# Optimization experiments

Hardware: AMD Instinct MI355X
Metric: run time of the kernel (lower is better)

## Reference

```python
import jax, jax.numpy as jnp
import numpy as np


def setup_inputs() -> dict:
    key = jax.random.key(0)
    k1, k2 = jax.random.split(key)
    B, C_in, H, Wd = 8, 64, 64, 64
    C_a = 32
    x = jax.random.normal(k1, (B, C_in, H, Wd), dtype=jnp.float32)
    # 1x1 conv == per-pixel linear map: weight [C_a, C_in], bias [C_a]
    W = jax.random.normal(k2, (C_a, C_in), dtype=jnp.float32) * (1.0 / np.sqrt(C_in))
    b = jnp.zeros((C_a,), dtype=jnp.float32)
    return {"x": x, "W": W, "b": b}


def reference(x, W, b):
    B, C, H, Wd = x.shape
    N = H * Wd
    # g = 1x1 conv: [B, C_a, H, W] -> flatten spatial -> [B, C_a, N]
    g = jnp.einsum('oc,bchw->bohw', W, x) + b[None, :, None, None]
    g = g.reshape(B, -1, N)
    # alpha[b, n, m] = softmax_m( sum_c g[b,c,n] * g[b,c,m] )  (unscaled)
    scores = jnp.einsum('bcn,bcm->bnm', g, g)
    alpha = jax.nn.softmax(scores, axis=2)
    # r[b, c, n] = sum_m alpha[b,n,m] * x[b,c,m]
    xf = x.reshape(B, C, N)
    r = jnp.einsum('bnm,bcm->bcn', alpha, xf)
    # residual (intended semantics of is_residual=True) + ReLU epilogue
    r = r + xf
    out = jax.nn.relu(r).reshape(B, C, H, Wd)
    return (out, alpha)
```

## Files before the change

kernel.cpp:

```cpp
#include <hip/hip_runtime.h>
#include <math.h>

#define BB 8
#define CC 64
#define NA 4096
#define KA 32
#define LOG2E 1.4426950408889634f

typedef short bfrag __attribute__((ext_vector_type(8)));
typedef int   i4    __attribute__((ext_vector_type(4)));
typedef float f4    __attribute__((ext_vector_type(4)));
typedef float f16v  __attribute__((ext_vector_type(16)));

__device__ __forceinline__ f16v mf(bfrag a, bfrag b, f16v c) {
    return __builtin_amdgcn_mfma_f32_32x32x16_bf16(a, b, c, 0, 0, 0);
}

__device__ __forceinline__ unsigned short bfrne(float f) {
    unsigned u = __builtin_bit_cast(unsigned, f);
    return (unsigned short)((u + 0x7FFFu + ((u >> 16) & 1u)) >> 16);
}
__device__ __forceinline__ unsigned pk2(float a, float b) {
    return (unsigned)bfrne(a) | ((unsigned)bfrne(b) << 16);
}
__device__ __forceinline__ float bf2f(unsigned short h) {
    unsigned u = ((unsigned)h) << 16;
    return __builtin_bit_cast(float, u);
}

__global__ __launch_bounds__(256) void k_g(const float* __restrict__ x,
                                           const float* __restrict__ W,
                                           const float* __restrict__ bias,
                                           short* __restrict__ ghi,
                                           short* __restrict__ glo,
                                           float* __restrict__ norms,
                                           int* __restrict__ gmaxi,
                                           float* __restrict__ lsum) {
    __shared__ float Wl[KA * CC];
    __shared__ float bl[KA];
    __shared__ float red[4];
    int tid = threadIdx.x;
    for (int i = tid; i < KA * CC; i += 256) Wl[i] = W[i];
    if (tid < KA) bl[tid] = bias[tid];
    __syncthreads();

    int b = blockIdx.y;
    int n = blockIdx.x * 256 + tid;

    float acc[KA];
#pragma unroll
    for (int k = 0; k < KA; k++) acc[k] = 0.f;

    const float* xp = x + (size_t)b * CC * NA + n;
#pragma unroll 4
    for (int c = 0; c < CC; c++) {
        float xv = xp[(size_t)c * NA];
#pragma unroll
        for (int k = 0; k < KA; k++) acc[k] = fmaf(Wl[k * CC + c], xv, acc[k]);
    }

    float ss = 0.f;
    unsigned ph[KA / 2], pl[KA / 2];
#pragma unroll
    for (int k = 0; k < KA; k += 2) {
        float v0 = acc[k] + bl[k];
        float v1 = acc[k + 1] + bl[k + 1];
        ss = fmaf(v0, v0, fmaf(v1, v1, ss));
        unsigned short h0 = bfrne(v0), h1 = bfrne(v1);
        float l0 = v0 - bf2f(h0), l1 = v1 - bf2f(h1);
        ph[k / 2] = (unsigned)h0 | ((unsigned)h1 << 16);
        pl[k / 2] = (unsigned)bfrne(l0) | ((unsigned)bfrne(l1) << 16);
    }
    float nrm = sqrtf(ss);
    norms[b * NA + n] = nrm;
    lsum[b * NA + n] = 0.f;

    size_t row = ((size_t)b * NA + n) * KA;
#pragma unroll
    for (int q = 0; q < 4; q++) {
        i4 vh = { (int)ph[4 * q], (int)ph[4 * q + 1], (int)ph[4 * q + 2], (int)ph[4 * q + 3] };
        i4 vl = { (int)pl[4 * q], (int)pl[4 * q + 1], (int)pl[4 * q + 2], (int)pl[4 * q + 3] };
        *(i4*)(ghi + row + q * 8) = vh;
        *(i4*)(glo + row + q * 8) = vl;
    }

    float m = nrm;
#pragma unroll
    for (int off = 1; off < 64; off <<= 1) m = fmaxf(m, __shfl_xor(m, off));
    if ((tid & 63) == 0) red[tid >> 6] = m;
    __syncthreads();
    if (tid == 0) {
        float bm = fmaxf(fmaxf(red[0], red[1]), fmaxf(red[2], red[3]));
        atomicMax(&gmaxi[b], __float_as_int(bm));
    }
}

__global__ __launch_bounds__(256) void k_xb(const float* __restrict__ x,
                                            short* __restrict__ xb2) {
    __shared__ float t[64][65];
    const int tid = threadIdx.x;
    const int b = blockIdx.y;
    const int m0 = blockIdx.x * 64;

    const int c0 = tid >> 4, m4 = (tid & 15) * 4;
#pragma unroll
    for (int p = 0; p < 4; p++) {
        int c = p * 16 + c0;
        f4 v = *(const f4*)(x + ((size_t)b * CC + c) * NA + m0 + m4);
        t[c][m4 + 0] = v[0];
        t[c][m4 + 1] = v[1];
        t[c][m4 + 2] = v[2];
        t[c][m4 + 3] = v[3];
    }
    __syncthreads();

    short* xo = xb2 + (size_t)b * CC * NA;
#pragma unroll
    for (int q = 0; q < 2; q++) {
        int idx = q * 256 + tid;
        int mgl = idx >> 6, c = idx & 63;
        i4 pkd;
#pragma unroll
        for (int j = 0; j < 4; j++)
            pkd[j] = (int)pk2(t[c][mgl * 8 + 2 * j], t[c][mgl * 8 + 2 * j + 1]);
        *(i4*)(xo + (size_t)(((m0 >> 3) + mgl) * 64 + c) * 8) = pkd;
    }
}

__global__ __launch_bounds__(256, 4) void k_den(const short* __restrict__ ghi,
                                                const short* __restrict__ glo,
                                                const float* __restrict__ norms,
                                                const int* __restrict__ gmaxi,
                                                float* __restrict__ lsum) {
    __shared__ float rowsum[4][32];
    const int tid = threadIdx.x;
    const int w = tid >> 6;
    const int l31 = tid & 31;
    const int hi = (tid >> 5) & 1;
    const int id = blockIdx.x;
    const int b = id & 7;
    const int rr = id >> 3;
    const int nb = rr & 127;
    const int mc = rr >> 7;
    const int n0 = nb * 32;

    const float gmax = __int_as_float(gmaxi[b]);
    const float C2 = -norms[b * NA + n0 + l31] * gmax * LOG2E;
    const short* gh = ghi + (size_t)b * NA * KA;
    const short* gl = glo + (size_t)b * NA * KA;

    bfrag Bh[2], Bl[2];
#pragma unroll
    for (int kt = 0; kt < 2; kt++) {
        size_t o = (size_t)(n0 + l31) * KA + kt * 16 + hi * 8;
        Bh[kt] = *(const bfrag*)(gh + o);
        Bl[kt] = *(const bfrag*)(gl + o);
    }

    float ls = 0.f;
#pragma unroll 2
    for (int i = 0; i < 8; i++) {
        const int m0 = (mc * 8 + i) * 128 + w * 32;
        bfrag Ah[2], Al[2];
#pragma unroll
        for (int kt = 0; kt < 2; kt++) {
            size_t o = (size_t)(m0 + l31) * KA + kt * 16 + hi * 8;
            Ah[kt] = *(const bfrag*)(gh + o);
            Al[kt] = *(const bfrag*)(gl + o);
        }
        f16v sA = {}, sB = {};
        sA = mf(Ah[0], Bh[0], sA); sA = mf(Ah[1], Bh[1], sA);
        sB = mf(Ah[0], Bl[0], sB); sB = mf(Ah[1], Bl[1], sB);
        sB = mf(Al[0], Bh[0], sB); sB = mf(Al[1], Bh[1], sB);
#pragma unroll
        for (int r = 0; r < 16; r++) ls += exp2f(fmaf(sA[r] + sB[r], LOG2E, C2));
    }
    ls += __shfl_xor(ls, 32);
    if (hi == 0) rowsum[w][l31] = ls;
    __syncthreads();
    if (tid < 32)
        atomicAdd(&lsum[b * NA + n0 + tid],
                  rowsum[0][tid] + rowsum[1][tid] + rowsum[2][tid] + rowsum[3][tid]);
}

__global__ __launch_bounds__(256, 2) void k_attn2(const float* __restrict__ x,
                                                  const short* __restrict__ ghi,
                                                  const short* __restrict__ glo,
                                                  const short* __restrict__ xb2,
                                                  const float* __restrict__ norms,
                                                  const int* __restrict__ gmaxi,
                                                  const float* __restrict__ lsum,
                                                  float* __restrict__ out,
                                                  float* __restrict__ alpha) {
    __shared__ __align__(16) char smem[2 * 32 * 256 * 4];
    float* ast = (float*)smem;

    const int tid = threadIdx.x;
    const int w = tid >> 6;
    const int l = tid & 63;
    const int l31 = tid & 31;
    const int hi = (tid >> 5) & 1;
    const int id = blockIdx.x;
    const int b = id & 7;
    const int n0 = (id >> 3) * 32;

    const float M = norms[b * NA + n0 + l31] * __int_as_float(gmaxi[b]);
    const float C2L = fmaf(-M, LOG2E, -__log2f(lsum[b * NA + n0 + l31]));

    const short* gh = ghi + (size_t)b * NA * KA;
    const short* gl = glo + (size_t)b * NA * KA;
    const short* xp = xb2 + (size_t)b * CC * NA;
    float* ap = alpha + (size_t)b * NA * NA;

    bfrag Bh[2], Bl[2];
#pragma unroll
    for (int kt = 0; kt < 2; kt++) {
        size_t o = (size_t)(n0 + l31) * KA + kt * 16 + hi * 8;
        Bh[kt] = *(const bfrag*)(gh + o);
        Bl[kt] = *(const bfrag*)(gl + o);
    }

    f16v pv0 = {}, pv1 = {};

    for (int it = 0; it < 16; ++it) {
        float* astb = ast + (it & 1) * 8192;

#pragma unroll
        for (int sub = 0; sub < 2; ++sub) {
            const int m0 = it * 256 + sub * 128 + w * 32;
            bfrag Ah[2], Al[2];
#pragma unroll
            for (int kt = 0; kt < 2; kt++) {
                size_t o = (size_t)(m0 + l31) * KA + kt * 16 + hi * 8;
                Ah[kt] = *(const bfrag*)(gh + o);
                Al[kt] = *(const bfrag*)(gl + o);
            }
            f16v sA = {}, sB = {};
            sA = mf(Ah[0], Bh[0], sA); sA = mf(Ah[1], Bh[1], sA);
            sB = mf(Ah[0], Bl[0], sB); sB = mf(Ah[1], Bl[1], sB);
            sB = mf(Al[0], Bh[0], sB); sB = mf(Al[1], Bh[1], sB);

            float a[16];
#pragma unroll
            for (int r = 0; r < 16; r++) a[r] = exp2f(fmaf(sA[r] + sB[r], LOG2E, C2L));

#pragma unroll
            for (int q = 0; q < 4; q++) {
                f4 v = { a[4 * q], a[4 * q + 1], a[4 * q + 2], a[4 * q + 3] };
                int phys = (w * 8 + 2 * q + hi) ^ (l31 & 7);
                *(f4*)&astb[l31 * 256 + sub * 128 + phys * 4] = v;
            }

            unsigned p0 = pk2(a[0], a[1]),   p1 = pk2(a[2], a[3]);
            unsigned p2 = pk2(a[4], a[5]),   p3 = pk2(a[6], a[7]);
            unsigned p4 = pk2(a[8], a[9]),   p5 = pk2(a[10], a[11]);
            unsigned p6 = pk2(a[12], a[13]), p7 = pk2(a[14], a[15]);
            asm("v_permlane32_swap_b32 %0, %1" : "+v"(p0), "+v"(p2));
            asm("v_permlane32_swap_b32 %0, %1" : "+v"(p1), "+v"(p3));
            asm("v_permlane32_swap_b32 %0, %1" : "+v"(p4), "+v"(p6));
            asm("v_permlane32_swap_b32 %0, %1" : "+v"(p5), "+v"(p7));
            i4 f0 = { (int)p0, (int)p1, (int)p2, (int)p3 };
            i4 f1 = { (int)p4, (int)p5, (int)p6, (int)p7 };
            bfrag pa0 = __builtin_bit_cast(bfrag, f0);
            bfrag pa1 = __builtin_bit_cast(bfrag, f1);

            const int mg = m0 >> 3;
            bfrag X00 = *(const bfrag*)(xp + (size_t)((mg + hi) * 64 + l31) * 8);
            bfrag X01 = *(const bfrag*)(xp + (size_t)((mg + 2 + hi) * 64 + l31) * 8);
            bfrag X10 = *(const bfrag*)(xp + (size_t)((mg + hi) * 64 + 32 + l31) * 8);
            bfrag X11 = *(const bfrag*)(xp + (size_t)((mg + 2 + hi) * 64 + 32 + l31) * 8);

            pv0 = mf(pa0, X00, pv0); pv0 = mf(pa1, X01, pv0);
            pv1 = mf(pa0, X10, pv1); pv1 = mf(pa1, X11, pv1);
        }

        __syncthreads();

#pragma unroll
        for (int e = 0; e < 8; e++) {
            int row = w * 8 + e;
            int c4 = l;
            int phys = (c4 & 31) ^ e;
            f4 v = *(const f4*)&astb[row * 256 + (c4 >> 5) * 128 + phys * 4];
            __builtin_nontemporal_store(v, (f4*)(ap + (size_t)(n0 + row) * NA + it * 256 + c4 * 4));
        }
    }
    __syncthreads();

    float (*pvr0)[CC + 1] = (float(*)[CC + 1])smem;
    float (*pvr1)[CC + 1] = (float(*)[CC + 1])(smem + 32 * (CC + 1) * 4);
    if (w >= 2) {
        float (*buf)[CC + 1] = (w == 2) ? pvr0 : pvr1;
#pragma unroll
        for (int r = 0; r < 16; r++) {
            int nl = (r & 3) + 8 * (r >> 2) + 4 * hi;
            buf[nl][l31]      = pv0[r];
            buf[nl][32 + l31] = pv1[r];
        }
    }
    __syncthreads();
    if (w < 2) {
        float (*buf)[CC + 1] = (w == 0) ? pvr0 : pvr1;
#pragma unroll
        for (int r = 0; r < 16; r++) {
            int nl = (r & 3) + 8 * (r >> 2) + 4 * hi;
            buf[nl][l31]      += pv0[r];
            buf[nl][32 + l31] += pv1[r];
        }
    }
    __syncthreads();

    const float* xr = x + (size_t)b * CC * NA + n0;
    float* op = out + (size_t)b * CC * NA + n0;
#pragma unroll
    for (int e = 0; e < 8; e++) {
        int idx = e * 256 + tid;
        int c = idx >> 5, n = idx & 31;
        float v = pvr0[n][c] + pvr1[n][c] + xr[(size_t)c * NA + n];
        op[(size_t)c * NA + n] = fmaxf(v, 0.f);
    }
}

extern "C" void kernel_launch(void* const* d_in, const int* in_sizes, int n_in,
                              void* d_out, int out_size, void* d_ws, size_t ws_size,
                              hipStream_t stream) {
    const float* x = (const float*)d_in[0];
    const float* W = (const float*)d_in[1];
    const float* bias = (const float*)d_in[2];

    float* out = (float*)d_out;
    float* alpha = out + (size_t)BB * CC * NA;

    short* ghi = (short*)d_ws;
    short* glo = ghi + (size_t)BB * NA * KA;
    short* xb2 = glo + (size_t)BB * NA * KA;
    float* norms = (float*)(xb2 + (size_t)BB * CC * NA);
    int*   gmaxi = (int*)(norms + (size_t)BB * NA);
    float* lsum  = (float*)(gmaxi + 8);

    k_g<<<dim3(NA / 256, BB), 256, 0, stream>>>(x, W, bias, ghi, glo, norms, gmaxi, lsum);
    k_xb<<<dim3(NA / 64, BB), 256, 0, stream>>>(x, xb2);
    k_den<<<4096, 256, 0, stream>>>(ghi, glo, norms, gmaxi, lsum);
    k_attn2<<<1024, 256, 0, stream>>>(x, ghi, glo, xb2, norms, gmaxi, lsum, out, alpha);
}
```

Before: 181.3 us.

## Software-pipeline A and X fragment loads across sub-tiles in attention kernel

The k_attn2 main loop now prefetches the g hi/lo fragments and bf16 x fragments for the next 128-column sub-tile into registers while the current sub-tile is computed, using two ping-pong register sets. This is meant to hide global load latency behind the MFMA and exp work. It also replaces __syncthreads with an inline s_waitcnt lgkmcnt(0) plus s_barrier, which skips waiting on outstanding global loads (vmcnt) so the prefetches can stay in flight across the barrier. The cost is higher register pressure under launch_bounds(256,2), which could force spills or lower occupancy.

```diff
diff --git a/kernel.cpp b/kernel.cpp
--- a/kernel.cpp
+++ b/kernel.cpp
@@ -183,6 +183,20 @@
                   rowsum[0][tid] + rowsum[1][tid] + rowsum[2][tid] + rowsum[3][tid]);
 }
 
+#define LOADA(dst, m0v) do { \
+    size_t _o = (size_t)((m0v) + l31) * KA + hi * 8; \
+    dst[0] = *(const bfrag*)(gh + _o); \
+    dst[1] = *(const bfrag*)(gh + _o + 16); \
+    dst[2] = *(const bfrag*)(gl + _o); \
+    dst[3] = *(const bfrag*)(gl + _o + 16); } while (0)
+
+#define LOADX(dst, m0v) do { \
+    const int _mg = (m0v) >> 3; \
+    dst[0] = *(const bfrag*)(xp + (size_t)((_mg + hi) * 64 + l31) * 8); \
+    dst[1] = *(const bfrag*)(xp + (size_t)((_mg + 2 + hi) * 64 + l31) * 8); \
+    dst[2] = *(const bfrag*)(xp + (size_t)((_mg + hi) * 64 + 32 + l31) * 8); \
+    dst[3] = *(const bfrag*)(xp + (size_t)((_mg + 2 + hi) * 64 + 32 + l31) * 8); } while (0)
+
 __global__ __launch_bounds__(256, 2) void k_attn2(const float* __restrict__ x,
                                                   const short* __restrict__ ghi,
                                                   const short* __restrict__ glo,
@@ -222,23 +236,21 @@
 
     f16v pv0 = {}, pv1 = {};
 
+    bfrag Af0[4], Af1[4], Xf0[4], Xf1[4];
+    LOADA(Af0, w * 32);
+    LOADX(Xf0, w * 32);
+
     for (int it = 0; it < 16; ++it) {
         float* astb = ast + (it & 1) * 8192;
-
-#pragma unroll
-        for (int sub = 0; sub < 2; ++sub) {
-            const int m0 = it * 256 + sub * 128 + w * 32;
-            bfrag Ah[2], Al[2];
-#pragma unroll
-            for (int kt = 0; kt < 2; kt++) {
-                size_t o = (size_t)(m0 + l31) * KA + kt * 16 + hi * 8;
-                Ah[kt] = *(const bfrag*)(gh + o);
-                Al[kt] = *(const bfrag*)(gl + o);
-            }
+        const int mb = it * 256 + w * 32;
+
+        LOADA(Af1, mb + 128);
+        LOADX(Xf1, mb + 128);
+        {
             f16v sA = {}, sB = {};
-            sA = mf(Ah[0], Bh[0], sA); sA = mf(Ah[1], Bh[1], sA);
-            sB = mf(Ah[0], Bl[0], sB); sB = mf(Ah[1], Bl[1], sB);
-            sB = mf(Al[0], Bh[0], sB); sB = mf(Al[1], Bh[1], sB);
+            sA = mf(Af0[0], Bh[0], sA); sA = mf(Af0[1], Bh[1], sA);
+            sB = mf(Af0[0], Bl[0], sB); sB = mf(Af0[1], Bl[1], sB);
+            sB = mf(Af0[2], Bh[0], sB); sB = mf(Af0[3], Bh[1], sB);
 
             float a[16];
 #pragma unroll
@@ -248,7 +260,7 @@
             for (int q = 0; q < 4; q++) {
                 f4 v = { a[4 * q], a[4 * q + 1], a[4 * q + 2], a[4 * q + 3] };
                 int phys = (w * 8 + 2 * q + hi) ^ (l31 & 7);
-                *(f4*)&astb[l31 * 256 + sub * 128 + phys * 4] = v;
+                *(f4*)&astb[l31 * 256 + phys * 4] = v;
             }
 
             unsigned p0 = pk2(a[0], a[1]),   p1 = pk2(a[2], a[3]);
@@ -264,17 +276,49 @@
             bfrag pa0 = __builtin_bit_cast(bfrag, f0);
             bfrag pa1 = __builtin_bit_cast(bfrag, f1);
 
-            const int mg = m0 >> 3;
-            bfrag X00 = *(const bfrag*)(xp + (size_t)((mg + hi) * 64 + l31) * 8);
-            bfrag X01 = *(const bfrag*)(xp + (size_t)((mg + 2 + hi) * 64 + l31) * 8);
-            bfrag X10 = *(const bfrag*)(xp + (size_t)((mg + hi) * 64 + 32 + l31) * 8);
-            bfrag X11 = *(const bfrag*)(xp + (size_t)((mg + 2 + hi) * 64 + 32 + l31) * 8);
-
-            pv0 = mf(pa0, X00, pv0); pv0 = mf(pa1, X01, pv0);
-            pv1 = mf(pa0, X10, pv1); pv1 = mf(pa1, X11, pv1);
-        }
-
-        __syncthreads();
+            pv0 = mf(pa0, Xf0[0], pv0); pv0 = mf(pa1, Xf0[1], pv0);
+            pv1 = mf(pa0, Xf0[2], pv1); pv1 = mf(pa1, Xf0[3], pv1);
+        }
+
+        if (it < 15) {
+            LOADA(Af0, mb + 256);
+            LOADX(Xf0, mb + 256);
+        }
+        {
+            f16v sA = {}, sB = {};
+            sA = mf(Af1[0], Bh[0], sA); sA = mf(Af1[1], Bh[1], sA);
+            sB = mf(Af1[0], Bl[0], sB); sB = mf(Af1[1], Bl[1], sB);
+            sB = mf(Af1[2], Bh[0], sB); sB = mf(Af1[3], Bh[1], sB);
+
+            float a[16];
+#pragma unroll
+            for (int r = 0; r < 16; r++) a[r] = exp2f(fmaf(sA[r] + sB[r], LOG2E, C2L));
+
+#pragma unroll
+            for (int q = 0; q < 4; q++) {
+                f4 v = { a[4 * q], a[4 * q + 1], a[4 * q + 2], a[4 * q + 3] };
+                int phys = (w * 8 + 2 * q + hi) ^ (l31 & 7);
+                *(f4*)&astb[l31 * 256 + 128 + phys * 4] = v;
+            }
+
+            unsigned p0 = pk2(a[0], a[1]),   p1 = pk2(a[2], a[3]);
+            unsigned p2 = pk2(a[4], a[5]),   p3 = pk2(a[6], a[7]);
+            unsigned p4 = pk2(a[8], a[9]),   p5 = pk2(a[10], a[11]);
+            unsigned p6 = pk2(a[12], a[13]), p7 = pk2(a[14], a[15]);
+            asm("v_permlane32_swap_b32 %0, %1" : "+v"(p0), "+v"(p2));
+            asm("v_permlane32_swap_b32 %0, %1" : "+v"(p1), "+v"(p3));
+            asm("v_permlane32_swap_b32 %0, %1" : "+v"(p4), "+v"(p6));
+            asm("v_permlane32_swap_b32 %0, %1" : "+v"(p5), "+v"(p7));
+            i4 f0 = { (int)p0, (int)p1, (int)p2, (int)p3 };
+            i4 f1 = { (int)p4, (int)p5, (int)p6, (int)p7 };
+            bfrag pa0 = __builtin_bit_cast(bfrag, f0);
+            bfrag pa1 = __builtin_bit_cast(bfrag, f1);
+
+            pv0 = mf(pa0, Xf1[0], pv0); pv0 = mf(pa1, Xf1[1], pv0);
+            pv1 = mf(pa0, Xf1[2], pv1); pv1 = mf(pa1, Xf1[3], pv1);
+        }
+
+        asm volatile("s_waitcnt lgkmcnt(0)\n\ts_barrier" ::: "memory");
 
 #pragma unroll
         for (int e = 0; e < 8; e++) {
```

Result: no change. 180.9 us (-0.2%).
